# Kernel optimization log

Measured on AMD Instinct MI355X. Metric: run time of the kernel, lower is better.

Reference implementation:

```python
import jax, jax.numpy as jnp
import numpy as np

VEC_DIM = 128   # D (also the per-head dim in this module)
HEADS = 8
PATCH = 4
WIN = 7
N_BATCH = 4
H_IMG = 448
W_IMG = 448


def _relative_index():
    # Swin-style relative position index, computed statically (matches torch code
    # which uses torch.meshgrid with default 'ij' indexing).
    coords = np.stack(np.meshgrid(np.arange(WIN), np.arange(WIN), indexing='ij'))  # [2,W,W]
    flat = coords.reshape(2, -1)                      # [2, W*W]
    rel = flat[:, :, None] - flat[:, None, :]         # [2, p, p]
    rel = rel.transpose(1, 2, 0).astype(np.int64)     # [p, p, 2]
    rel[:, :, 0] += WIN - 1
    rel[:, :, 1] += WIN - 1
    rel[:, :, 1] *= 2 * WIN - 1
    return rel.sum(-1)                                # [p, p], values in [0, (2W-1)^2)

REL_IDX = jnp.asarray(_relative_index())


def setup_inputs() -> dict:
    key = jax.random.key(0)
    ks = jax.random.split(key, 8)
    P = (H_IMG // PATCH) * (W_IMG // PATCH)  # 12544
    D, H = VEC_DIM, HEADS
    s = 0.02
    return {
        'x': jax.random.normal(ks[0], (N_BATCH, D, P), jnp.float32),
        'Wq': jax.random.normal(ks[1], (H * D, D), jnp.float32) * s,
        'bq': jnp.zeros((H * D,), jnp.float32),
        'Wk': jax.random.normal(ks[2], (H * D, D), jnp.float32) * s,
        'bk': jnp.zeros((H * D,), jnp.float32),
        'Wv': jax.random.normal(ks[3], (H * D, D), jnp.float32) * s,
        'bv': jnp.zeros((H * D,), jnp.float32),
        'Wo': jax.random.normal(ks[4], (D, H * D), jnp.float32) * s,
        'bo': jnp.zeros((D,), jnp.float32),
        'pos_code': jax.random.normal(ks[5], ((2 * WIN - 1) ** 2, H), jnp.float32) * s,
        'h': H_IMG,
        'w': W_IMG,
    }


def reference(x, Wq, bq, Wk, bk, Wv, bv, Wo, bo, pos_code, h, w):
    N, D, P = x.shape
    H = HEADS
    ch, cw = h // PATCH, w // PATCH
    nh, nw = ch // WIN, cw // WIN            # windows per axis
    p = WIN * WIN                            # tokens per window

    def emb(W, b):
        # pointwise Conv1d: [N,D,P] -> [N,H*D,P] -> [N,H,D,P]
        return (jnp.einsum('od,ndp->nop', W, x) + b[None, :, None]).reshape(N, H, D, P)

    def partition(e):
        # [N,H,D,P] -> [N,H,win_num,D,p]
        e = e.reshape(N, H, D, nh, WIN, nw, WIN)
        return e.transpose(0, 1, 3, 5, 2, 4, 6).reshape(N, H, nh * nw, D, p)

    q = partition(emb(Wq, bq))
    k = partition(emb(Wk, bk))
    v = partition(emb(Wv, bv))

    # attn[n,h,w,i,j] = sum_d k[n,h,w,d,i] * q[n,h,w,d,j], scaled
    attn = jnp.einsum('nhwdi,nhwdj->nhwij', k, q) / (D ** 0.5)
    bias = pos_code[REL_IDX].transpose(2, 0, 1)          # [H, p, p]
    attn = attn + bias[None, :, None, :, :]
    weights = jax.nn.softmax(attn, axis=3)               # softmax over key index i

    # out[n,h,w,d,j] = sum_i v[n,h,w,d,i] * weights[n,h,w,i,j]
    out = jnp.einsum('nhwdi,nhwij->nhwdj', v, weights)

    # window merge: [N,H,win_num,D,p] -> [N,H*D,P]
    out = out.reshape(N, H, nh, nw, D, WIN, WIN)
    out = out.transpose(0, 1, 4, 2, 5, 3, 6).reshape(N, H * D, P)

    return jnp.einsum('od,ndp->nop', Wo, out) + bo[None, :, None]
```

## Files before the change

kernel.cpp:

```cpp
#include <hip/hip_runtime.h>
#include <hip/hip_bf16.h>

typedef unsigned short u16;
typedef unsigned int u32;
typedef __attribute__((ext_vector_type(8))) short bf16x8;
typedef __attribute__((ext_vector_type(4))) float f32x4;
typedef __attribute__((ext_vector_type(2))) unsigned int u32x2;

#define NBATCH 4
#define DDIM   128
#define NHEAD  8
#define PTOT   12544
#define CWID   112
#define NTOK   49
#define PSTR   68
#define SCALE  0.08838834764831845f

#define BUFSZ   16384
#define OFF_US  8192
#define OFF_PL  32768
#define OFF_PCF 36100
#define OFF_CS  38804
#define LDS_TOT 39828

__device__ __forceinline__ float bf2f(u16 u) {
    union { u32 i; float f; } x; x.i = ((u32)u) << 16; return x.f;
}
__device__ __forceinline__ u16 f2bf(float f) {
    union { float f; u32 u; } v; v.f = f;
    return (u16)((v.u + 0x7fffu + ((v.u >> 16) & 1u)) >> 16);
}
__device__ __forceinline__ u32 pk2(float a, float b) {
    union { __hip_bfloat162 h; u32 u; } c;
    float2 t; t.x = a; t.y = b;
    c.h = __float22bfloat162_rn(t);
    return c.u;
}
__device__ __forceinline__ int swz128(int row, int col) {
    return row * 128 + ((((col >> 3) ^ (row & 15)) & 15) << 3) + (col & 7);
}

#define WS_WC   131072
#define WS_F32  262144

__global__ void __launch_bounds__(256) prep(
    const float* __restrict__ Wq, const float* __restrict__ Wk,
    const float* __restrict__ Wv, const float* __restrict__ Wo,
    const float* __restrict__ bq, const float* __restrict__ bk,
    const float* __restrict__ bv, u16* __restrict__ ws)
{
    __shared__ u16 lm[18432];
    const int tid = threadIdx.x;
    const int bb  = blockIdx.x;
    const int b   = bb >> 3;
    const int sub = bb & 7;
    const bool isG = (b >= 8);
    const int h = b & 7;
    const int r0 = sub * 16;
    float* fb = (float*)(ws + WS_F32);

    if (!isG) {
        for (int idx = tid; idx < 2048; idx += 256) {
            const int lr = idx >> 7, dh = idx & 127;
            lm[swz128(lr, dh)] = f2bf(Wo[(r0 + lr) * 1024 + h * 128 + dh]);
        }
        for (int idx = tid; idx < 16384; idx += 256) {
            const int dh = idx >> 7, d = idx & 127;
            lm[2048 + swz128(d, dh)] = f2bf(Wv[(h * 128 + dh) * 128 + d]);
        }
        if (sub == 0 && tid < 128) {
            float s = 0.f;
            for (int dh = 0; dh < 128; ++dh)
                s += Wo[tid * 1024 + h * 128 + dh] * bv[h * 128 + dh];
            fb[h * 128 + tid] = s;
        }
    } else {
        for (int idx = tid; idx < 2048; idx += 256) {
            const int dh = idx >> 4, lr = idx & 15;
            lm[swz128(lr, dh)] = f2bf(Wk[(h * 128 + dh) * 128 + r0 + lr]);
        }
        for (int idx = tid; idx < 16384; idx += 256) {
            const int dh = idx >> 7, dp = idx & 127;
            lm[2048 + swz128(dp, dh)] = f2bf(Wq[(h * 128 + dh) * 128 + dp]);
        }
        if (sub == 0 && tid < 128) {
            float r = 0.f, m = 0.f;
            for (int dh = 0; dh < 128; ++dh) {
                r += bk[h * 128 + dh] * Wq[(h * 128 + dh) * 128 + tid];
                m += Wk[(h * 128 + dh) * 128 + tid] * bq[h * 128 + dh];
            }
            fb[1024 + h * 128 + tid] = r * SCALE;
            fb[2048 + h * 128 + tid] = m * SCALE;
        }
        if (sub == 0 && tid == 0) {
            float s = 0.f;
            for (int dh = 0; dh < 128; ++dh) s += bk[h * 128 + dh] * bq[h * 128 + dh];
            fb[3072 + h] = s * SCALE;
        }
    }
    __syncthreads();

    const int w = tid >> 6, lane = tid & 63, quad = lane >> 4, lid = lane & 15;
    const f32x4 z4 = {0.f, 0.f, 0.f, 0.f};
    u16* dst = ws + (isG ? 0 : WS_WC) + h * 16384;
    const float gs = isG ? SCALE : 1.0f;
    bf16x8 A[4];
    #pragma unroll
    for (int kt = 0; kt < 4; ++kt)
        A[kt] = *(const bf16x8*)(lm + swz128(lid, kt * 32 + quad * 8));
    #pragma unroll
    for (int ntl = 0; ntl < 2; ++ntl) {
        const int nt = 2 * w + ntl;
        f32x4 acc = z4;
        #pragma unroll
        for (int kt = 0; kt < 4; ++kt) {
            bf16x8 B = *(const bf16x8*)(lm + 2048 + swz128(nt * 16 + lid, kt * 32 + quad * 8));
            acc = __builtin_amdgcn_mfma_f32_16x16x32_bf16(A[kt], B, acc, 0, 0, 0);
        }
        #pragma unroll
        for (int r = 0; r < 4; ++r) {
            const int row = r0 + quad * 4 + r, col = nt * 16 + lid;
            if (isG) dst[col * 128 + row] = f2bf(acc[r] * gs);
            else     dst[row * 128 + col] = f2bf(acc[r]);
        }
    }
}

#define STAGE_B(WW) \
    _Pragma("unroll") \
    for (int mt = 0; mt < 4; ++mt) { \
        _Pragma("unroll") \
        for (int kt = 0; kt < 4; ++kt) { \
            bf16x8 Abf = *(const bf16x8*)(tsb + (mt * 16 + lid) * 128 + ((((kt * 4 + quad) ^ lid) & 15) << 3)); \
            S[mt] = __builtin_amdgcn_mfma_f32_16x16x32_bf16(Abf, xfrag[WW][kt], S[mt], 0, 0, 0); \
        } \
    }

__global__ void __launch_bounds__(256, 2)
winattn(const float* __restrict__ xg, const u16* __restrict__ ws,
        const float* __restrict__ bo, const float* __restrict__ posf,
        float* __restrict__ out)
{
    __shared__ __align__(16) u16 sm[LDS_TOT];
    u16* xw  = sm;
    u16* pl  = sm + OFF_PL;
    float* pcf = (float*)(sm + OFF_PCF);
    float* cs  = (float*)(sm + OFF_CS);

    const int tid  = threadIdx.x;
    const int w    = tid >> 6;
    const int lane = tid & 63;
    const int quad = lane >> 4;
    const int lid  = lane & 15;
    const int bx   = blockIdx.x;
    const int n    = bx >> 8;
    const int win  = bx & 255;
    const int pbase = (win >> 4) * 7 * CWID + (win & 15) * 7;

    const bf16x8 zf = {0,0,0,0,0,0,0,0};
    const f32x4  z4 = {0.f,0.f,0.f,0.f};

    const u16* Gt  = ws;
    const u16* Wcw = ws + WS_WC;
    const float* fb  = (const float*)(ws + WS_F32);
    const float* bcv = fb;
    const float* rP  = fb + 1024;
    const float* MP  = fb + 2048;
    const float* sP  = fb + 3072;

    for (int i = tid; i < 169 * NHEAD; i += 256) pcf[i] = posf[i];
    const float* xn = xg + n * DDIM * PTOT;
    for (int idx = tid; idx < DDIM * NTOK; idx += 256) {
        int d = idx / NTOK;
        int t = idx - d * NTOK;
        int a = t / 7, b = t - a * 7;
        xw[swz128(t, d)] = f2bf(xn[d * PTOT + pbase + a * CWID + b]);
    }
    __syncthreads();

    bf16x8 xfrag[4][4];
    #pragma unroll
    for (int mt = 0; mt < 4; ++mt)
        #pragma unroll
        for (int kt = 0; kt < 4; ++kt)
            xfrag[mt][kt] = (mt * 16 + lid < NTOK)
                ? *(const bf16x8*)(xw + swz128(mt * 16 + lid, kt * 32 + quad * 8)) : zf;
    const int j = 16 * w + lid;

    bf16x8 GA[2][4];
    #pragma unroll
    for (int mtl = 0; mtl < 2; ++mtl)
        #pragma unroll
        for (int kt = 0; kt < 4; ++kt)
            GA[mtl][kt] = *(const bf16x8*)(Gt + ((2 * w + mtl) * 16 + lid) * 128 + kt * 32 + quad * 8);

    for (int hh = w; hh < NHEAD; hh += 4) {
        const float sh = sP[hh];
        #pragma unroll
        for (int mt = 0; mt < 4; ++mt) {
            float c = 0.f;
            #pragma unroll
            for (int kt = 0; kt < 4; ++kt)
                #pragma unroll
                for (int jj = 0; jj < 8; ++jj)
                    c += bf2f((u16)xfrag[mt][kt][jj]) * MP[hh * 128 + kt * 32 + quad * 8 + jj];
            c += __shfl_xor(c, 16);
            c += __shfl_xor(c, 32);
            if (quad == 0) cs[hh * 64 + mt * 16 + lid] = c + sh;
        }
    }
    __syncthreads();

    f32x4 outacc[8];
    #pragma unroll
    for (int nt = 0; nt < 8; ++nt) outacc[nt] = z4;

    const int jc = j < NTOK ? j : NTOK - 1;
    const int aj = jc / 7, bj = jc - aj * 7;

    #pragma unroll 2
    for (int h = 0; h < NHEAD; ++h) {
        u16* tsb = sm + (h & 1) * BUFSZ;
        u16* usb = tsb + OFF_US;

        #pragma unroll
        for (int mtl = 0; mtl < 2; ++mtl) {
            const int mt = 2 * w + mtl;
            const f32x4 rb = *(const f32x4*)(rP + h * 128 + mt * 16 + quad * 4);
            const int dpb = mt * 16 + quad * 4;
            #pragma unroll
            for (int nt = 0; nt < 4; ++nt) {
                f32x4 acc = z4;
                #pragma unroll
                for (int kt = 0; kt < 4; ++kt)
                    acc = __builtin_amdgcn_mfma_f32_16x16x32_bf16(GA[mtl][kt], xfrag[nt][kt], acc, 0, 0, 0);
                const int i = nt * 16 + lid;
                u32x2 pkv;
                pkv.x = pk2(acc[0] + rb[0], acc[1] + rb[1]);
                pkv.y = pk2(acc[2] + rb[2], acc[3] + rb[3]);
                *(u32x2*)(tsb + i * 128 + ((((dpb >> 3) ^ (i & 15)) & 15) << 3) + (dpb & 7)) = pkv;
            }
        }
        #pragma unroll
        for (int ntl = 0; ntl < 2; ++ntl) {
            const int nt = 2 * w + ntl;
            bf16x8 B[4];
            #pragma unroll
            for (int kt = 0; kt < 4; ++kt)
                B[kt] = *(const bf16x8*)(Wcw + h * 16384 + (nt * 16 + lid) * 128 + kt * 32 + quad * 8);
            const int dd = nt * 16 + lid;
            const float bb = bcv[h * 128 + dd];
            #pragma unroll
            for (int mt = 0; mt < 4; ++mt) {
                f32x4 acc = z4;
                #pragma unroll
                for (int kt = 0; kt < 4; ++kt)
                    acc = __builtin_amdgcn_mfma_f32_16x16x32_bf16(xfrag[mt][kt], B[kt], acc, 0, 0, 0);
                const int ib = mt * 16 + quad * 4;
                u32x2 pkv;
                pkv.x = pk2(acc[0] + bb, acc[1] + bb);
                pkv.y = pk2(acc[2] + bb, acc[3] + bb);
                *(u32x2*)(usb + dd * 64 + ((((ib >> 3) ^ (dd & 7)) & 7) << 3) + (ib & 7)) = pkv;
            }
        }
        __syncthreads();

        {
            const int hn = (h + 1) & 7;
            #pragma unroll
            for (int mtl = 0; mtl < 2; ++mtl)
                #pragma unroll
                for (int kt = 0; kt < 4; ++kt)
                    GA[mtl][kt] = *(const bf16x8*)(Gt + hn * 16384 + ((2 * w + mtl) * 16 + lid) * 128 + kt * 32 + quad * 8);
        }

        f32x4 S[4];
        #pragma unroll
        for (int mt = 0; mt < 4; ++mt) S[mt] = z4;
        if      (w == 0) { STAGE_B(0) }
        else if (w == 1) { STAGE_B(1) }
        else if (w == 2) { STAGE_B(2) }
        else             { STAGE_B(3) }

        float sv[4][4];
        float ssum = 0.f;
        #pragma unroll
        for (int mt = 0; mt < 4; ++mt)
            #pragma unroll
            for (int r = 0; r < 4; ++r) {
                const int ii = mt * 16 + quad * 4 + r;
                float e;
                if (ii < NTOK) {
                    const int ai = ii / 7, bi = ii - ai * 7;
                    const int rel = (ai - aj + 6) + 13 * (bi - bj + 6);
                    e = __expf(S[mt][r] + cs[h * 64 + ii] + pcf[rel * NHEAD + h]);
                } else {
                    e = 0.0f;
                }
                sv[mt][r] = e;
                ssum += e;
            }
        ssum += __shfl_xor(ssum, 16);
        ssum += __shfl_xor(ssum, 32);
        const float inv = 1.0f / ssum;
        if (j < NTOK) {
            #pragma unroll
            for (int mt = 0; mt < 4; ++mt) {
                u32x2 pkv;
                pkv.x = pk2(sv[mt][0] * inv, sv[mt][1] * inv);
                pkv.y = pk2(sv[mt][2] * inv, sv[mt][3] * inv);
                *(u32x2*)(pl + j * PSTR + mt * 16 + quad * 4) = pkv;
            }
        }
        __threadfence_block();

        #pragma unroll
        for (int kt = 0; kt < 2; ++kt) {
            union { bf16x8 v; u32 u[4]; } Af;
            #pragma unroll
            for (int q2 = 0; q2 < 4; ++q2)
                Af.u[q2] = *(const u32*)(pl + jc * PSTR + kt * 32 + quad * 8 + 2 * q2);
            #pragma unroll
            for (int nt = 0; nt < 8; ++nt) {
                const int dd = nt * 16 + lid;
                bf16x8 Bu = *(const bf16x8*)(usb + dd * 64 + ((((kt * 4 + quad) ^ (dd & 7)) & 7) << 3));
                outacc[nt] = __builtin_amdgcn_mfma_f32_16x16x32_bf16(Af.v, Bu, outacc[nt], 0, 0, 0);
            }
        }
    }

    float* outp = out + n * DDIM * PTOT;
    #pragma unroll
    for (int nt = 0; nt < 8; ++nt) {
        const int dd = nt * 16 + lid;
        const float bov = bo[dd];
        #pragma unroll
        for (int r = 0; r < 4; ++r) {
            const int jj = 16 * w + quad * 4 + r;
            if (jj < NTOK) {
                const int a = jj / 7, b = jj - a * 7;
                outp[dd * PTOT + pbase + a * CWID + b] = outacc[nt][r] + bov;
            }
        }
    }
}

extern "C" void kernel_launch(void* const* d_in, const int* in_sizes, int n_in,
                              void* d_out, int out_size, void* d_ws, size_t ws_size,
                              hipStream_t stream) {
    (void)in_sizes; (void)n_in; (void)ws_size; (void)out_size;
    prep<<<128, 256, 0, stream>>>((const float*)d_in[1], (const float*)d_in[3],
                                  (const float*)d_in[5], (const float*)d_in[7],
                                  (const float*)d_in[2], (const float*)d_in[4],
                                  (const float*)d_in[6], (u16*)d_ws);
    winattn<<<NBATCH * 256, 256, 0, stream>>>(
        (const float*)d_in[0], (const u16*)d_ws,
        (const float*)d_in[8], (const float*)d_in[9], (float*)d_out);
}
```

Before: 227.1 us.

## Prefetch next-head weight fragments, remap blocks across XCDs, add MFMA priority hints

Moves the per-head Wc weight fragment loads out of the MFMA loop into registers that are prefetched for the next head during softmax, so global load latency overlaps compute. Block indices are remapped so that consecutive windows of the same batch land on the same XCD, which may improve L2 locality. It wraps the MFMA phases in s_setprio hints and replaces the block fence with an explicit lgkmcnt wait. The extra prefetch registers raise register pressure and could hurt occupancy at the two-block launch bound.

```diff
diff --git a/kernel.cpp b/kernel.cpp
--- a/kernel.cpp
+++ b/kernel.cpp
@@ -152,9 +152,11 @@
     const int lane = tid & 63;
     const int quad = lane >> 4;
     const int lid  = lane & 15;
-    const int bx   = blockIdx.x;
-    const int n    = bx >> 8;
-    const int win  = bx & 255;
+    const int bx0  = blockIdx.x;
+    const int xcd  = bx0 & 7;
+    const int idx0 = bx0 >> 3;
+    const int n    = idx0 >> 5;
+    const int win  = xcd * 32 + (idx0 & 31);
     const int pbase = (win >> 4) * 7 * CWID + (win & 15) * 7;
 
     const bf16x8 zf = {0,0,0,0,0,0,0,0};
@@ -187,12 +189,14 @@
                 ? *(const bf16x8*)(xw + swz128(mt * 16 + lid, kt * 32 + quad * 8)) : zf;
     const int j = 16 * w + lid;
 
-    bf16x8 GA[2][4];
+    bf16x8 GA[2][4], WBn[2][4];
     #pragma unroll
     for (int mtl = 0; mtl < 2; ++mtl)
         #pragma unroll
-        for (int kt = 0; kt < 4; ++kt)
-            GA[mtl][kt] = *(const bf16x8*)(Gt + ((2 * w + mtl) * 16 + lid) * 128 + kt * 32 + quad * 8);
+        for (int kt = 0; kt < 4; ++kt) {
+            GA[mtl][kt]  = *(const bf16x8*)(Gt  + ((2 * w + mtl) * 16 + lid) * 128 + kt * 32 + quad * 8);
+            WBn[mtl][kt] = *(const bf16x8*)(Wcw + ((2 * w + mtl) * 16 + lid) * 128 + kt * 32 + quad * 8);
+        }
 
     for (int hh = w; hh < NHEAD; hh += 4) {
         const float sh = sP[hh];
@@ -223,6 +227,7 @@
         u16* tsb = sm + (h & 1) * BUFSZ;
         u16* usb = tsb + OFF_US;
 
+        __builtin_amdgcn_s_setprio(1);
         #pragma unroll
         for (int mtl = 0; mtl < 2; ++mtl) {
             const int mt = 2 * w + mtl;
@@ -244,10 +249,6 @@
         #pragma unroll
         for (int ntl = 0; ntl < 2; ++ntl) {
             const int nt = 2 * w + ntl;
-            bf16x8 B[4];
-            #pragma unroll
-            for (int kt = 0; kt < 4; ++kt)
-                B[kt] = *(const bf16x8*)(Wcw + h * 16384 + (nt * 16 + lid) * 128 + kt * 32 + quad * 8);
             const int dd = nt * 16 + lid;
             const float bb = bcv[h * 128 + dd];
             #pragma unroll
@@ -255,7 +256,7 @@
                 f32x4 acc = z4;
                 #pragma unroll
                 for (int kt = 0; kt < 4; ++kt)
-                    acc = __builtin_amdgcn_mfma_f32_16x16x32_bf16(xfrag[mt][kt], B[kt], acc, 0, 0, 0);
+                    acc = __builtin_amdgcn_mfma_f32_16x16x32_bf16(xfrag[mt][kt], WBn[ntl][kt], acc, 0, 0, 0);
                 const int ib = mt * 16 + quad * 4;
                 u32x2 pkv;
                 pkv.x = pk2(acc[0] + bb, acc[1] + bb);
@@ -263,6 +264,7 @@
                 *(u32x2*)(usb + dd * 64 + ((((ib >> 3) ^ (dd & 7)) & 7) << 3) + (ib & 7)) = pkv;
             }
         }
+        __builtin_amdgcn_s_setprio(0);
         __syncthreads();
 
         {
@@ -277,10 +279,12 @@
         f32x4 S[4];
         #pragma unroll
         for (int mt = 0; mt < 4; ++mt) S[mt] = z4;
+        __builtin_amdgcn_s_setprio(1);
         if      (w == 0) { STAGE_B(0) }
         else if (w == 1) { STAGE_B(1) }
         else if (w == 2) { STAGE_B(2) }
         else             { STAGE_B(3) }
+        __builtin_amdgcn_s_setprio(0);
 
         float sv[4][4];
         float ssum = 0.f;
@@ -312,8 +316,19 @@
                 *(u32x2*)(pl + j * PSTR + mt * 16 + quad * 4) = pkv;
             }
         }
-        __threadfence_block();
-
+
+        {
+            const int hn = (h + 1) & 7;
+            #pragma unroll
+            for (int ntl = 0; ntl < 2; ++ntl)
+                #pragma unroll
+                for (int kt = 0; kt < 4; ++kt)
+                    WBn[ntl][kt] = *(const bf16x8*)(Wcw + hn * 16384 + ((2 * w + ntl) * 16 + lid) * 128 + kt * 32 + quad * 8);
+        }
+
+        asm volatile("s_waitcnt lgkmcnt(0)" ::: "memory");
+
+        __builtin_amdgcn_s_setprio(1);
         #pragma unroll
         for (int kt = 0; kt < 2; ++kt) {
             union { bf16x8 v; u32 u[4]; } Af;
@@ -327,6 +342,7 @@
                 outacc[nt] = __builtin_amdgcn_mfma_f32_16x16x32_bf16(Af.v, Bu, outacc[nt], 0, 0, 0);
             }
         }
+        __builtin_amdgcn_s_setprio(0);
     }
 
     float* outp = out + n * DDIM * PTOT;
```

Measured after the change: 220.8 us. 1.03x faster.
